# Kernel optimization log

Hardware: AMD Instinct MI355X
Metric: run time of the kernel (lower is better)

## Reference

```python
import jax, jax.numpy as jnp
import numpy as np

N, D, K = 524288, 256, 64
ALPHA = 1.0


def setup_inputs() -> dict:
    key = jax.random.key(0)
    k1, k2 = jax.random.split(key)
    inputs = jax.random.normal(k1, (N, D), dtype=jnp.float32)
    clusters = jax.random.normal(k2, (K, D), dtype=jnp.float32)  # glorot-init stand-in
    return {"inputs": inputs, "clusters": clusters}


def reference(inputs, clusters):
    # Squared euclidean distance ||x - c||^2 via GEMM expansion: same math as
    # sum((x[:,None,:] - c[None,:,:])**2, -1) without the (N,K,D) intermediate.
    x2 = jnp.sum(inputs * inputs, axis=1, keepdims=True)          # (N,1)
    c2 = jnp.sum(clusters * clusters, axis=1)                     # (K,)
    d2 = x2 + c2 - 2.0 * (inputs @ clusters.T)                    # (N,K)
    d2 = jnp.maximum(d2, 0.0)                                     # numeric guard
    q = 1.0 / (1.0 + d2 / ALPHA)                                  # Student-t kernel
    q = q ** ((ALPHA + 1.0) / 2.0)
    return q / jnp.sum(q, axis=1, keepdims=True)                  # row-normalize
```

## Files before the change

### kernel.cpp

```cpp
#include <hip/hip_runtime.h>
#include <hip/hip_bf16.h>

#define NPTS 524288
#define DIM 256
#define KC 64

typedef __attribute__((ext_vector_type(8))) short bf16x8;
typedef __attribute__((ext_vector_type(4))) float f32x4;

typedef __attribute__((address_space(1))) const unsigned int GUI;
typedef __attribute__((address_space(3))) unsigned int LUI;

static __device__ __forceinline__ void gload16(const void* g, void* l) {
  __builtin_amdgcn_global_load_lds((GUI*)g, (LUI*)l, 16, 0, 0);
}

static __device__ __forceinline__ ushort f32_to_bf16_rne(float f) {
  unsigned int b = __builtin_bit_cast(unsigned int, f);
  b += 0x7FFFu + ((b >> 16) & 1u);
  return (ushort)(b >> 16);
}

static __device__ __forceinline__ short f2bf(float f) {
  return __builtin_bit_cast(short, __float2bfloat16(f));
}

__global__ void prep_clusters(const float* __restrict__ C,
                              char* __restrict__ cb,
                              float* __restrict__ c2) {
  const int w = threadIdx.x >> 6;
  const int lane = threadIdx.x & 63;
  const int k = blockIdx.x * 8 + w * 2 + (lane >> 5);
  const int m = lane & 31;
  const float* src = C + k * DIM + m * 8;
  float4 u0 = ((const float4*)src)[0];
  float4 u1 = ((const float4*)src)[1];
  float vv[8] = {u0.x, u0.y, u0.z, u0.w, u1.x, u1.y, u1.z, u1.w};
  float s = 0.f;
  bf16x8 h;
#pragma unroll
  for (int j = 0; j < 8; ++j) {
    s = fmaf(vv[j], vv[j], s);
    h[j] = (short)f32_to_bf16_rne(vv[j]);
  }
  s += __shfl_xor(s, 1);
  s += __shfl_xor(s, 2);
  s += __shfl_xor(s, 4);
  s += __shfl_xor(s, 8);
  s += __shfl_xor(s, 16);
  const int slot = 16 * (k & 3) + (k >> 2);
  const int off = slot * 512 + ((m ^ (slot & 7)) << 4);
  *(bf16x8*)(cb + off) = h;
  if (m == 0) c2[k] = s;
}

__global__ __launch_bounds__(256, 4)
void cluster_q(const float* __restrict__ A, const char* __restrict__ cb,
               const float* __restrict__ c2, float* __restrict__ out) {
  __shared__ char lds[32768];
  const int tid = threadIdx.x;
  const int lane = tid & 63;
  const int w = tid >> 6;
  const int l15 = lane & 15;
  const int g = lane >> 4;
  const long brow = (long)blockIdx.x * 64;

  const char* Ap = (const char*)A + (brow + w * 16 + l15) * 1024 + g * 32;

  float4 b0a = *(const float4*)(Ap + 0 * 128);
  float4 b0b = *(const float4*)(Ap + 0 * 128 + 16);
  float4 b1a = *(const float4*)(Ap + 1 * 128);
  float4 b1b = *(const float4*)(Ap + 1 * 128 + 16);

  {
    const char* src = cb + w * 8192 + lane * 16;
    char* dst = lds + w * 8192;
#pragma unroll
    for (int i = 0; i < 8; ++i)
      gload16(src + i * 1024, dst + i * 1024);
  }
  __syncthreads();

  f32x4 acc[4];
#pragma unroll
  for (int t = 0; t < 4; ++t) acc[t] = (f32x4){0.f, 0.f, 0.f, 0.f};
  float x2l = 0.f;
  float4 b2a, b2b;

#define KSTEP(ks, CA, CB, PA, PB)                                            \
  do {                                                                       \
    float vv[8] = {CA.x, CA.y, CA.z, CA.w, CB.x, CB.y, CB.z, CB.w};          \
    if ((ks) + 2 < 8) {                                                      \
      PA = *(const float4*)(Ap + ((ks) + 2) * 128);                          \
      PB = *(const float4*)(Ap + ((ks) + 2) * 128 + 16);                     \
    }                                                                        \
    bf16x8 af;                                                               \
    _Pragma("unroll") for (int j = 0; j < 8; ++j) {                          \
      x2l = fmaf(vv[j], vv[j], x2l);                                         \
      af[j] = f2bf(vv[j]);                                                   \
    }                                                                        \
    _Pragma("unroll") for (int t = 0; t < 4; ++t) {                          \
      int slot = l15 + 16 * t;                                               \
      bf16x8 bf = *(const bf16x8*)(lds + slot * 512 +                        \
                                   ((((ks) * 4 + g) ^ (slot & 7)) << 4));    \
      acc[t] = __builtin_amdgcn_mfma_f32_16x16x32_bf16(af, bf, acc[t], 0, 0, 0); \
    }                                                                        \
  } while (0)

  KSTEP(0, b0a, b0b, b2a, b2b);
  KSTEP(1, b1a, b1b, b0a, b0b);
  KSTEP(2, b2a, b2b, b1a, b1b);
  KSTEP(3, b0a, b0b, b2a, b2b);
  KSTEP(4, b1a, b1b, b0a, b0b);
  KSTEP(5, b2a, b2b, b1a, b1b);
  KSTEP(6, b0a, b0b, b0a, b0b);
  KSTEP(7, b1a, b1b, b0a, b0b);
#undef KSTEP

  x2l += __shfl_xor(x2l, 16);
  x2l += __shfl_xor(x2l, 32);
  float x2r[4];
#pragma unroll
  for (int r = 0; r < 4; ++r) x2r[r] = __shfl(x2l, g * 4 + r);

  float4 c2v = *(const float4*)(c2 + 4 * l15);
  float c2a[4] = {c2v.x, c2v.y, c2v.z, c2v.w};

  float qv[4][4];
  float rsum[4] = {0.f, 0.f, 0.f, 0.f};
#pragma unroll
  for (int t = 0; t < 4; ++t) {
#pragma unroll
    for (int r = 0; r < 4; ++r) {
      float d2 = fmaxf(x2r[r] + c2a[t] - 2.0f * acc[t][r], 0.f);
      float qq = __builtin_amdgcn_rcpf(1.0f + d2);
      qv[t][r] = qq;
      rsum[r] += qq;
    }
  }
#pragma unroll
  for (int r = 0; r < 4; ++r) {
    rsum[r] += __shfl_xor(rsum[r], 1);
    rsum[r] += __shfl_xor(rsum[r], 2);
    rsum[r] += __shfl_xor(rsum[r], 4);
    rsum[r] += __shfl_xor(rsum[r], 8);
    float inv = __builtin_amdgcn_rcpf(rsum[r]);
    long orow = brow + w * 16 + g * 4 + r;
    float4 o4 = {qv[0][r] * inv, qv[1][r] * inv, qv[2][r] * inv, qv[3][r] * inv};
    *(float4*)(out + orow * 64 + 4 * l15) = o4;
  }
}

extern "C" void kernel_launch(void* const* d_in, const int* in_sizes, int n_in,
                              void* d_out, int out_size, void* d_ws, size_t ws_size,
                              hipStream_t stream) {
  const float* inputs = (const float*)d_in[0];
  const float* clusters = (const float*)d_in[1];
  float* out = (float*)d_out;

  char* cb = (char*)d_ws;
  float* c2 = (float*)((char*)d_ws + 32768);

  prep_clusters<<<8, 256, 0, stream>>>(clusters, cb, c2);
  cluster_q<<<NPTS / 64, 256, 0, stream>>>(inputs, cb, c2, out);
}
```

Before: 131.2 us.

## Issue all input loads upfront with nontemporal hints and nontemporal output stores

The rolling two-deep register prefetch of input rows is replaced by issuing all 16 float4 loads per thread at kernel start, using nontemporal loads. The cluster LDS copy is waited on with a manual vmcnt wait and raw barrier instead of __syncthreads, so the input loads stay in flight across the barrier. Output stores become nontemporal. This aims to raise memory-level parallelism and avoid cache pollution on a streaming workload, at the cost of more VGPRs and a hand-counted waitcnt that relies on load ordering.

```diff
diff --git a/kernel.cpp b/kernel.cpp
--- a/kernel.cpp
+++ b/kernel.cpp
@@ -23,6 +23,10 @@
 
 static __device__ __forceinline__ short f2bf(float f) {
   return __builtin_bit_cast(short, __float2bfloat16(f));
+}
+
+static __device__ __forceinline__ f32x4 ntld(const void* p) {
+  return __builtin_nontemporal_load((const f32x4*)p);
 }
 
 __global__ void prep_clusters(const float* __restrict__ C,
@@ -67,11 +71,6 @@
 
   const char* Ap = (const char*)A + (brow + w * 16 + l15) * 1024 + g * 32;
 
-  float4 b0a = *(const float4*)(Ap + 0 * 128);
-  float4 b0b = *(const float4*)(Ap + 0 * 128 + 16);
-  float4 b1a = *(const float4*)(Ap + 1 * 128);
-  float4 b1b = *(const float4*)(Ap + 1 * 128 + 16);
-
   {
     const char* src = cb + w * 8192 + lane * 16;
     char* dst = lds + w * 8192;
@@ -79,25 +78,32 @@
     for (int i = 0; i < 8; ++i)
       gload16(src + i * 1024, dst + i * 1024);
   }
-  __syncthreads();
+  __builtin_amdgcn_sched_barrier(0);
+
+  f32x4 av[16];
+#pragma unroll
+  for (int k2 = 0; k2 < 16; ++k2)
+    av[k2] = ntld(Ap + (k2 >> 1) * 128 + (k2 & 1) * 16);
+  __builtin_amdgcn_sched_barrier(0);
+
+  asm volatile("s_waitcnt vmcnt(16)" ::: "memory");
+  __builtin_amdgcn_s_barrier();
+  __builtin_amdgcn_sched_barrier(0);
 
   f32x4 acc[4];
 #pragma unroll
   for (int t = 0; t < 4; ++t) acc[t] = (f32x4){0.f, 0.f, 0.f, 0.f};
   float x2l = 0.f;
-  float4 b2a, b2b;
 
-#define KSTEP(ks, CA, CB, PA, PB)                                            \
+#define KSTEP(ks)                                                            \
   do {                                                                       \
-    float vv[8] = {CA.x, CA.y, CA.z, CA.w, CB.x, CB.y, CB.z, CB.w};          \
-    if ((ks) + 2 < 8) {                                                      \
-      PA = *(const float4*)(Ap + ((ks) + 2) * 128);                          \
-      PB = *(const float4*)(Ap + ((ks) + 2) * 128 + 16);                     \
-    }                                                                        \
+    f32x4 CA = av[2 * (ks)];                                                 \
+    f32x4 CB = av[2 * (ks) + 1];                                             \
+    float vv[8] = {CA[0], CA[1], CA[2], CA[3], CB[0], CB[1], CB[2], CB[3]};  \
     bf16x8 af;                                                               \
-    _Pragma("unroll") for (int j = 0; j < 8; ++j) {                          \
-      x2l = fmaf(vv[j], vv[j], x2l);                                         \
-      af[j] = f2bf(vv[j]);                                                   \
+    _Pragma("unroll") for (int j2 = 0; j2 < 8; ++j2) {                       \
+      x2l = fmaf(vv[j2], vv[j2], x2l);                                       \
+      af[j2] = f2bf(vv[j2]);                                                 \
     }                                                                        \
     _Pragma("unroll") for (int t = 0; t < 4; ++t) {                          \
       int slot = l15 + 16 * t;                                               \
@@ -107,14 +113,8 @@
     }                                                                        \
   } while (0)
 
-  KSTEP(0, b0a, b0b, b2a, b2b);
-  KSTEP(1, b1a, b1b, b0a, b0b);
-  KSTEP(2, b2a, b2b, b1a, b1b);
-  KSTEP(3, b0a, b0b, b2a, b2b);
-  KSTEP(4, b1a, b1b, b0a, b0b);
-  KSTEP(5, b2a, b2b, b1a, b1b);
-  KSTEP(6, b0a, b0b, b0a, b0b);
-  KSTEP(7, b1a, b1b, b0a, b0b);
+  KSTEP(0); KSTEP(1); KSTEP(2); KSTEP(3);
+  KSTEP(4); KSTEP(5); KSTEP(6); KSTEP(7);
 #undef KSTEP
 
   x2l += __shfl_xor(x2l, 16);
@@ -146,8 +146,8 @@
     rsum[r] += __shfl_xor(rsum[r], 8);
     float inv = __builtin_amdgcn_rcpf(rsum[r]);
     long orow = brow + w * 16 + g * 4 + r;
-    float4 o4 = {qv[0][r] * inv, qv[1][r] * inv, qv[2][r] * inv, qv[3][r] * inv};
-    *(float4*)(out + orow * 64 + 4 * l15) = o4;
+    f32x4 o4 = {qv[0][r] * inv, qv[1][r] * inv, qv[2][r] * inv, qv[3][r] * inv};
+    __builtin_nontemporal_store(o4, (f32x4*)(out + orow * 64 + 4 * l15));
   }
 }
 
```

Result: no change. 133.5 us (+1.7%).

## Fuse cluster preprocessing into main kernel, converting clusters to bf16 in LDS per block

Applied to the files above, without the earlier changes.

Removes the separate prep_clusters launch and its workspace round trip. Each block now reads the fp32 cluster matrix, computes squared norms, converts to bf16 and writes the swizzled layout straight into LDS, with c2 kept in shared memory. This saves a kernel launch and the dependency between the two kernels, but every one of 8192 blocks now re-reads 64 KB of fp32 clusters (from L2) and does redundant conversion work. The A-tile loads are also moved after the barrier, so they no longer overlap with the cluster staging.

```diff
diff --git a/kernel.cpp b/kernel.cpp
--- a/kernel.cpp
+++ b/kernel.cpp
@@ -8,56 +8,15 @@
 typedef __attribute__((ext_vector_type(8))) short bf16x8;
 typedef __attribute__((ext_vector_type(4))) float f32x4;
 
-typedef __attribute__((address_space(1))) const unsigned int GUI;
-typedef __attribute__((address_space(3))) unsigned int LUI;
-
-static __device__ __forceinline__ void gload16(const void* g, void* l) {
-  __builtin_amdgcn_global_load_lds((GUI*)g, (LUI*)l, 16, 0, 0);
-}
-
-static __device__ __forceinline__ ushort f32_to_bf16_rne(float f) {
-  unsigned int b = __builtin_bit_cast(unsigned int, f);
-  b += 0x7FFFu + ((b >> 16) & 1u);
-  return (ushort)(b >> 16);
-}
-
 static __device__ __forceinline__ short f2bf(float f) {
   return __builtin_bit_cast(short, __float2bfloat16(f));
 }
 
-__global__ void prep_clusters(const float* __restrict__ C,
-                              char* __restrict__ cb,
-                              float* __restrict__ c2) {
-  const int w = threadIdx.x >> 6;
-  const int lane = threadIdx.x & 63;
-  const int k = blockIdx.x * 8 + w * 2 + (lane >> 5);
-  const int m = lane & 31;
-  const float* src = C + k * DIM + m * 8;
-  float4 u0 = ((const float4*)src)[0];
-  float4 u1 = ((const float4*)src)[1];
-  float vv[8] = {u0.x, u0.y, u0.z, u0.w, u1.x, u1.y, u1.z, u1.w};
-  float s = 0.f;
-  bf16x8 h;
-#pragma unroll
-  for (int j = 0; j < 8; ++j) {
-    s = fmaf(vv[j], vv[j], s);
-    h[j] = (short)f32_to_bf16_rne(vv[j]);
-  }
-  s += __shfl_xor(s, 1);
-  s += __shfl_xor(s, 2);
-  s += __shfl_xor(s, 4);
-  s += __shfl_xor(s, 8);
-  s += __shfl_xor(s, 16);
-  const int slot = 16 * (k & 3) + (k >> 2);
-  const int off = slot * 512 + ((m ^ (slot & 7)) << 4);
-  *(bf16x8*)(cb + off) = h;
-  if (m == 0) c2[k] = s;
-}
-
 __global__ __launch_bounds__(256, 4)
-void cluster_q(const float* __restrict__ A, const char* __restrict__ cb,
-               const float* __restrict__ c2, float* __restrict__ out) {
-  __shared__ char lds[32768];
+void cluster_q(const float* __restrict__ A, const float* __restrict__ C,
+               float* __restrict__ out) {
+  __shared__ __align__(16) char lds[33024];
+  float* c2s = (float*)(lds + 32768);
   const int tid = threadIdx.x;
   const int lane = tid & 63;
   const int w = tid >> 6;
@@ -67,25 +26,42 @@
 
   const char* Ap = (const char*)A + (brow + w * 16 + l15) * 1024 + g * 32;
 
+  {
+    const int k = tid >> 2;
+    const int qt = tid & 3;
+    const int slot = 16 * (k & 3) + (k >> 2);
+    const float4* src = (const float4*)(C + k * DIM + qt * 64);
+    float s = 0.f;
+#pragma unroll
+    for (int i = 0; i < 8; ++i) {
+      float4 u0 = src[2 * i];
+      float4 u1 = src[2 * i + 1];
+      float vv[8] = {u0.x, u0.y, u0.z, u0.w, u1.x, u1.y, u1.z, u1.w};
+      bf16x8 h;
+#pragma unroll
+      for (int j2 = 0; j2 < 8; ++j2) {
+        s = fmaf(vv[j2], vv[j2], s);
+        h[j2] = f2bf(vv[j2]);
+      }
+      const int m = qt * 8 + i;
+      *(bf16x8*)(lds + slot * 512 + ((m ^ (slot & 7)) << 4)) = h;
+    }
+    s += __shfl_xor(s, 1);
+    s += __shfl_xor(s, 2);
+    if (qt == 0) c2s[k] = s;
+  }
+  __syncthreads();
+
   float4 b0a = *(const float4*)(Ap + 0 * 128);
   float4 b0b = *(const float4*)(Ap + 0 * 128 + 16);
   float4 b1a = *(const float4*)(Ap + 1 * 128);
   float4 b1b = *(const float4*)(Ap + 1 * 128 + 16);
-
-  {
-    const char* src = cb + w * 8192 + lane * 16;
-    char* dst = lds + w * 8192;
-#pragma unroll
-    for (int i = 0; i < 8; ++i)
-      gload16(src + i * 1024, dst + i * 1024);
-  }
-  __syncthreads();
+  float4 b2a, b2b;
 
   f32x4 acc[4];
 #pragma unroll
   for (int t = 0; t < 4; ++t) acc[t] = (f32x4){0.f, 0.f, 0.f, 0.f};
   float x2l = 0.f;
-  float4 b2a, b2b;
 
 #define KSTEP(ks, CA, CB, PA, PB)                                            \
   do {                                                                       \
@@ -95,9 +71,9 @@
       PB = *(const float4*)(Ap + ((ks) + 2) * 128 + 16);                     \
     }                                                                        \
     bf16x8 af;                                                               \
-    _Pragma("unroll") for (int j = 0; j < 8; ++j) {                          \
-      x2l = fmaf(vv[j], vv[j], x2l);                                         \
-      af[j] = f2bf(vv[j]);                                                   \
+    _Pragma("unroll") for (int j2 = 0; j2 < 8; ++j2) {                       \
+      x2l = fmaf(vv[j2], vv[j2], x2l);                                       \
+      af[j2] = f2bf(vv[j2]);                                                 \
     }                                                                        \
     _Pragma("unroll") for (int t = 0; t < 4; ++t) {                          \
       int slot = l15 + 16 * t;                                               \
@@ -123,7 +99,7 @@
 #pragma unroll
   for (int r = 0; r < 4; ++r) x2r[r] = __shfl(x2l, g * 4 + r);
 
-  float4 c2v = *(const float4*)(c2 + 4 * l15);
+  float4 c2v = *(const float4*)(c2s + 4 * l15);
   float c2a[4] = {c2v.x, c2v.y, c2v.z, c2v.w};
 
   float qv[4][4];
@@ -157,10 +133,5 @@
   const float* inputs = (const float*)d_in[0];
   const float* clusters = (const float*)d_in[1];
   float* out = (float*)d_out;
-
-  char* cb = (char*)d_ws;
-  float* c2 = (float*)((char*)d_ws + 32768);
-
-  prep_clusters<<<8, 256, 0, stream>>>(clusters, cb, c2);
-  cluster_q<<<NPTS / 64, 256, 0, stream>>>(inputs, cb, c2, out);
+  cluster_q<<<NPTS / 64, 256, 0, stream>>>(inputs, clusters, out);
 }
```

Measured after the change: 156.9 us. 19.6% more time.
